# Optimization experiments

Measured on AMD Instinct MI355X. Metric: run time of the kernel, lower is better.

Reference implementation:

```python
import jax, jax.numpy as jnp
import numpy as np

B = 64            # batch of graphs
E = 8978          # edge-simplices per graph (nodes of the Hodge-1 graph)
E2 = E // 2       # after Graclus pair-pooling
K = 4             # Laguerre polynomial order
DEG = 16          # avg degree of the (edge-)adjacency
SLOPE = 0.33      # LeakyReLU negative slope
EPS = 1e-5        # BatchNorm eps


def _make_edges(rng, b, n, deg):
    # block-diagonal batched edge list: each graph only connects within itself
    offs = np.repeat(np.arange(b, dtype=np.int64) * n, n * deg)
    dst = np.tile(np.repeat(np.arange(n, dtype=np.int64), deg), b) + offs
    src = rng.integers(0, n, size=b * n * deg) + offs
    return np.stack([src, dst]).astype(np.int32)


def setup_inputs() -> dict:
    rng = np.random.default_rng(0)
    ks = jax.random.split(jax.random.key(0), 12)
    N1 = B * E
    ei1 = _make_edges(rng, B, E, DEG)
    ei2 = _make_edges(rng, B, E2, DEG)
    return {
        "x_s": jax.random.normal(ks[0], (N1, 1), jnp.float32),
        "edge_index_s": jnp.asarray(ei1),
        "edge_weight_s": jax.random.uniform(ks[1], (ei1.shape[1],), jnp.float32) * (2.0 / DEG),
        "edge_index_s1": jnp.asarray(ei2),
        "edge_weight_s1": jax.random.uniform(ks[2], (ei2.shape[1],), jnp.float32) * (2.0 / DEG),
        "W0": jax.random.normal(ks[3], (K, 1, 32), jnp.float32) * 0.3,
        "b0": jnp.zeros((32,), jnp.float32),
        "g0": jnp.ones((32,), jnp.float32),
        "be0": jnp.zeros((32,), jnp.float32),
        "W1": jax.random.normal(ks[4], (K, 32, 32), jnp.float32) * 0.1,
        "b1": jnp.zeros((32,), jnp.float32),
        "g1": jnp.ones((32,), jnp.float32),
        "be1": jnp.zeros((32,), jnp.float32),
        "W2": jax.random.normal(ks[5], (K, 32, 1), jnp.float32) * 0.1,
        "b2": jnp.zeros((1,), jnp.float32),
        "g2": jnp.ones((1,), jnp.float32),
        "be2": jnp.zeros((1,), jnp.float32),
        "lin1_W": jax.random.normal(ks[6], (E2, 256), jnp.float32) * 0.02,
        "lin1_b": jnp.zeros((256,), jnp.float32),
        "bn1_g": jnp.ones((256,), jnp.float32),
        "bn1_b": jnp.zeros((256,), jnp.float32),
        "lin2_W": jax.random.normal(ks[7], (256, 128), jnp.float32) * 0.06,
        "lin2_b": jnp.zeros((128,), jnp.float32),
        "bn2_g": jnp.ones((128,), jnp.float32),
        "bn2_b": jnp.zeros((128,), jnp.float32),
        "lin3_W": jax.random.normal(ks[8], (128, 1), jnp.float32) * 0.09,
        "lin3_b": jnp.zeros((1,), jnp.float32),
    }


def _laguerre_layer(x, src, dst, ew, W, b, gamma, beta, n):
    """HodgeLaguerreConv (K-order Laguerre recurrence over sparse L) + BatchNorm + LeakyReLU."""
    def matvec(v):  # (L v)[i] = sum_j w_ij v[j]
        return jax.ops.segment_sum(ew[:, None] * v[src], dst, num_segments=n)
    Tp = x                      # L_0(L) x = x
    out = Tp @ W[0]
    Tc = x - matvec(x)          # L_1(L) x = x - L x
    out = out + Tc @ W[1]
    for k in range(1, K - 1):   # L_{k+1} = ((2k+1-L) L_k - k L_{k-1}) / (k+1)
        Tn = ((2 * k + 1) * Tc - matvec(Tc) - k * Tp) / (k + 1)
        out = out + Tn @ W[k + 1]
        Tp, Tc = Tc, Tn
    out = out + b
    out = gamma * (out - out.mean(0)) * jax.lax.rsqrt(out.var(0) + EPS) + beta
    return jnp.where(out > 0, out, SLOPE * out)


def _bn(h, g, b):
    return g * (h - h.mean(0)) * jax.lax.rsqrt(h.var(0) + EPS) + b


def reference(x_s, edge_index_s, edge_weight_s, edge_index_s1, edge_weight_s1,
              W0, b0, g0, be0, W1, b1, g1, be1, W2, b2, g2, be2,
              lin1_W, lin1_b, bn1_g, bn1_b, lin2_W, lin2_b, bn2_g, bn2_b,
              lin3_W, lin3_b):
    N1, N2 = B * E, B * E2
    x = _laguerre_layer(x_s, edge_index_s[0], edge_index_s[1], edge_weight_s,
                        W0, b0, g0, be0, N1)
    # Graclus pooling: merge matched node pairs by max over features
    x = x.reshape(B, E2, 2, x.shape[-1]).max(axis=2).reshape(N2, -1)
    x = _laguerre_layer(x, edge_index_s1[0], edge_index_s1[1], edge_weight_s1,
                        W1, b1, g1, be1, N2)
    x = _laguerre_layer(x, edge_index_s1[0], edge_index_s1[1], edge_weight_s1,
                        W2, b2, g2, be2, N2)
    x = x.reshape(B, E2)        # last conv has 1 channel
    h = jax.nn.relu(_bn(x @ lin1_W + lin1_b, bn1_g, bn1_b))
    h = jax.nn.relu(_bn(h @ lin2_W + lin2_b, bn2_g, bn2_b))
    return h @ lin3_W + lin3_b  # [B, num_classes=1]
```

## Files before the change

### kernel.cpp

```cpp
#include <hip/hip_runtime.h>
#include <cstdint>

#define SLOPE 0.33f

static constexpr int B_   = 64;
static constexpr int E1_  = 8978;
static constexpr int E2_  = 4489;
static constexpr int N1_  = B_ * E1_;
static constexpr int N2_  = B_ * E2_;
static constexpr int DEG_ = 16;
static constexpr int QTR_ = 2245;
static constexpr int QTR2_ = 1123;
static constexpr int MVGRID = (N2_ * 32) / 256;
static constexpr int PROJ_GRID = (N2_ + 511) / 512;
static constexpr double EPS_ = 1e-5;

__device__ __forceinline__ float lrelu(float v) { return v > 0.f ? v : SLOPE * v; }
__device__ __forceinline__ float dot4(float4 a, float4 b) {
  return a.x * b.x + a.y * b.y + a.z * b.z + a.w * b.w;
}

__global__ __launch_bounds__(256) void k0_mv1(const float* __restrict__ x,
    const int* __restrict__ src, const float* __restrict__ ew, float* __restrict__ T1) {
  __shared__ float sx[E1_];
  int g = blockIdx.x >> 2, q = blockIdx.x & 3;
  int gbase = g * E1_;
  for (int j = threadIdx.x; j < E1_; j += 256) sx[j] = x[gbase + j];
  __syncthreads();
  int start = q * QTR_, end = min(start + QTR_, E1_);
  for (int i = start + (int)threadIdx.x; i < end; i += 256) {
    int node = gbase + i;
    const int4* s4 = (const int4*)(src + (size_t)node * DEG_);
    const float4* w4 = (const float4*)(ew + (size_t)node * DEG_);
    float acc = 0.f;
#pragma unroll
    for (int j = 0; j < 4; ++j) {
      int4 s = s4[j]; float4 w = w4[j];
      acc += w.x * sx[s.x - gbase] + w.y * sx[s.y - gbase]
           + w.z * sx[s.z - gbase] + w.w * sx[s.w - gbase];
    }
    T1[node] = sx[i] - acc;
  }
}

__global__ __launch_bounds__(256) void k0_mv2(const float* __restrict__ x,
    const int* __restrict__ src, const float* __restrict__ ew,
    const float* __restrict__ T1, float* __restrict__ T2) {
  __shared__ float sT[E1_];
  int g = blockIdx.x >> 2, q = blockIdx.x & 3;
  int gbase = g * E1_;
  for (int j = threadIdx.x; j < E1_; j += 256) sT[j] = T1[gbase + j];
  __syncthreads();
  int start = q * QTR_, end = min(start + QTR_, E1_);
  for (int i = start + (int)threadIdx.x; i < end; i += 256) {
    int node = gbase + i;
    const int4* s4 = (const int4*)(src + (size_t)node * DEG_);
    const float4* w4 = (const float4*)(ew + (size_t)node * DEG_);
    float acc = 0.f;
#pragma unroll
    for (int j = 0; j < 4; ++j) {
      int4 s = s4[j]; float4 w = w4[j];
      acc += w.x * sT[s.x - gbase] + w.y * sT[s.y - gbase]
           + w.z * sT[s.z - gbase] + w.w * sT[s.w - gbase];
    }
    T2[node] = (3.f * sT[i] - acc - x[node]) * 0.5f;
  }
}

__global__ __launch_bounds__(256) void k0_mv3(const float* __restrict__ x,
    const int* __restrict__ src, const float* __restrict__ ew,
    const float* __restrict__ T1, const float* __restrict__ T2,
    float* __restrict__ T3, double* mom) {
  __shared__ float sT[E1_];
  __shared__ double sred[4 * 14];
  int g = blockIdx.x >> 2, q = blockIdx.x & 3;
  int gbase = g * E1_;
  for (int j = threadIdx.x; j < E1_; j += 256) sT[j] = T2[gbase + j];
  __syncthreads();
  double m[14];
#pragma unroll
  for (int j = 0; j < 14; ++j) m[j] = 0.0;
  int start = q * QTR_, end = min(start + QTR_, E1_);
  for (int i = start + (int)threadIdx.x; i < end; i += 256) {
    int node = gbase + i;
    const int4* s4 = (const int4*)(src + (size_t)node * DEG_);
    const float4* w4 = (const float4*)(ew + (size_t)node * DEG_);
    float acc = 0.f;
#pragma unroll
    for (int j = 0; j < 4; ++j) {
      int4 s = s4[j]; float4 w = w4[j];
      acc += w.x * sT[s.x - gbase] + w.y * sT[s.y - gbase]
           + w.z * sT[s.z - gbase] + w.w * sT[s.w - gbase];
    }
    float t1 = T1[node];
    float t2 = sT[i];
    float t3 = (5.f * t2 - acc - 2.f * t1) * (1.f / 3.f);
    T3[node] = t3;
    double d0 = x[node], d1 = t1, d2 = t2, d3 = t3;
    m[0] += d0; m[1] += d1; m[2] += d2; m[3] += d3;
    m[4] += d0 * d0; m[5] += d0 * d1; m[6] += d0 * d2; m[7] += d0 * d3;
    m[8] += d1 * d1; m[9] += d1 * d2; m[10] += d1 * d3;
    m[11] += d2 * d2; m[12] += d2 * d3; m[13] += d3 * d3;
  }
  int lane = threadIdx.x & 63, wid = threadIdx.x >> 6;
#pragma unroll
  for (int j = 0; j < 14; ++j) {
    double v = m[j];
    for (int o = 32; o; o >>= 1) v += __shfl_down(v, o);
    if (lane == 0) sred[wid * 14 + j] = v;
  }
  __syncthreads();
  if (threadIdx.x < 14) {
    double s = sred[threadIdx.x] + sred[14 + threadIdx.x] + sred[28 + threadIdx.x] + sred[42 + threadIdx.x];
    atomicAdd(&mom[threadIdx.x], s);
  }
}

__global__ void k0_params(const double* __restrict__ mom, const float* __restrict__ W0,
    const float* __restrict__ g0, const float* __restrict__ be0,
    float* __restrict__ scale0, float* __restrict__ shiftE0) {
  int c = threadIdx.x;
  if (c >= 32) return;
  double inv = 1.0 / (double)N1_;
  double mm[4];
#pragma unroll
  for (int k = 0; k < 4; ++k) mm[k] = mom[k] * inv;
  double M[4][4];
  M[0][0] = mom[4] * inv;  M[0][1] = mom[5] * inv;  M[0][2] = mom[6] * inv;  M[0][3] = mom[7] * inv;
  M[1][1] = mom[8] * inv;  M[1][2] = mom[9] * inv;  M[1][3] = mom[10] * inv;
  M[2][2] = mom[11] * inv; M[2][3] = mom[12] * inv; M[3][3] = mom[13] * inv;
  M[1][0] = M[0][1]; M[2][0] = M[0][2]; M[3][0] = M[0][3];
  M[2][1] = M[1][2]; M[3][1] = M[1][3]; M[3][2] = M[2][3];
  double w[4];
#pragma unroll
  for (int k = 0; k < 4; ++k) w[k] = W0[k * 32 + c];
  double mean = 0.0;
#pragma unroll
  for (int k = 0; k < 4; ++k) mean += w[k] * mm[k];
  double e2 = 0.0;
#pragma unroll
  for (int k = 0; k < 4; ++k)
#pragma unroll
    for (int l = 0; l < 4; ++l) e2 += M[k][l] * w[k] * w[l];
  double var = e2 - mean * mean;
  double sc = (double)g0[c] / sqrt(var + EPS_);
  scale0[c] = (float)sc;
  shiftE0[c] = (float)((double)be0[c] - sc * mean);
}

__global__ __launch_bounds__(256) void k0_pool(const float* __restrict__ x,
    const float* __restrict__ T1, const float* __restrict__ T2, const float* __restrict__ T3,
    const float* __restrict__ W0, const float* __restrict__ scale0,
    const float* __restrict__ shiftE0, float* __restrict__ x1) {
  int gid = blockIdx.x * 256 + threadIdx.x;
  int grp = gid >> 5, c = gid & 31;
  if (grp >= N2_) return;
  int b = grp / E2_, j = grp - b * E2_;
  int ga = b * E1_ + 2 * j, gb = ga + 1;
  float w0 = W0[c], w1 = W0[32 + c], w2 = W0[64 + c], w3 = W0[96 + c];
  float da = x[ga] * w0 + T1[ga] * w1 + T2[ga] * w2 + T3[ga] * w3;
  float db = x[gb] * w0 + T1[gb] * w1 + T2[gb] * w2 + T3[gb] * w3;
  float sc = scale0[c], sh = shiftE0[c];
  float ya = lrelu(sc * da + sh), yb = lrelu(sc * db + sh);
  x1[grp * 32 + c] = fmaxf(ya, yb);
}

__global__ __launch_bounds__(256) void k1_projall(const float* __restrict__ X,
    const float* __restrict__ W1, float4* __restrict__ P4) {
  __shared__ float4 Wl[128 * 8];
  const float4 cfs[4] = { {0.f, 0.f, 0.f, -1.f / 6.f},
                          {0.f, 0.f, 0.5f, 1.5f},
                          {0.f, -1.f, -2.f, -3.f},
                          {1.f, 1.f, 1.f, 1.f} };
  for (int e = threadIdx.x; e < 1024; e += 256) {
    int o = e >> 3, qq = e & 7;
    int j = o >> 5, cp = o & 31;
    float4 cf = cfs[j];
    float4 w;
    {
      const float* wp = W1 + (4 * qq + 0) * 32 + cp;
      w.x = cf.x * wp[0] + cf.y * wp[1024] + cf.z * wp[2048] + cf.w * wp[3072];
    }
    {
      const float* wp = W1 + (4 * qq + 1) * 32 + cp;
      w.y = cf.x * wp[0] + cf.y * wp[1024] + cf.z * wp[2048] + cf.w * wp[3072];
    }
    {
      const float* wp = W1 + (4 * qq + 2) * 32 + cp;
      w.z = cf.x * wp[0] + cf.y * wp[1024] + cf.z * wp[2048] + cf.w * wp[3072];
    }
    {
      const float* wp = W1 + (4 * qq + 3) * 32 + cp;
      w.w = cf.x * wp[0] + cf.y * wp[1024] + cf.z * wp[2048] + cf.w * wp[3072];
    }
    Wl[e] = w;
  }
  __syncthreads();
  int rA = blockIdx.x * 512 + threadIdx.x;
  int rB = rA + 256;
  bool okA = rA < N2_, okB = rB < N2_;
  if (!okA) return;
  float4 xA[8], xB[8];
  {
    const float4* pa = (const float4*)(X + (size_t)rA * 32);
#pragma unroll
    for (int t = 0; t < 8; ++t) xA[t] = pa[t];
  }
  if (okB) {
    const float4* pb = (const float4*)(X + (size_t)rB * 32);
#pragma unroll
    for (int t = 0; t < 8; ++t) xB[t] = pb[t];
  } else {
#pragma unroll
    for (int t = 0; t < 8; ++t) xB[t] = {0.f, 0.f, 0.f, 0.f};
  }
  for (int oq = 0; oq < 32; ++oq) {
    float4 aA = {0.f, 0.f, 0.f, 0.f}, aB = {0.f, 0.f, 0.f, 0.f};
    const float4* wr = Wl + oq * 32;
#pragma unroll
    for (int qq = 0; qq < 8; ++qq) {
      float4 w0 = wr[0 * 8 + qq];
      float4 w1 = wr[1 * 8 + qq];
      float4 w2 = wr[2 * 8 + qq];
      float4 w3 = wr[3 * 8 + qq];
      float4 xa = xA[qq], xb = xB[qq];
      aA.x += dot4(xa, w0); aA.y += dot4(xa, w1); aA.z += dot4(xa, w2); aA.w += dot4(xa, w3);
      aB.x += dot4(xb, w0); aB.y += dot4(xb, w1); aB.z += dot4(xb, w2); aB.w += dot4(xb, w3);
    }
    P4[(size_t)oq * N2_ + rA] = aA;
    if (okB) P4[(size_t)oq * N2_ + rB] = aB;
  }
}

__global__ __launch_bounds__(1024) void k1_chain(const float4* __restrict__ P4,
    float4* __restrict__ O4, const int* __restrict__ src,
    const float* __restrict__ ew, double* st) {
  __shared__ float4 bA[E2_], bB[E2_];
  __shared__ float sacc[8];
  int v = (blockIdx.x & 7) * 64 + (blockIdx.x >> 3);
  int g = v >> 3, cg = v & 7;
  int gbase = g * E2_;
  int tid = threadIdx.x;
  if (tid < 8) sacc[tid] = 0.f;
  {
    const float4* sp = P4 + (size_t)cg * N2_ + gbase;
    for (int i = tid; i < E2_; i += 1024) bA[i] = sp[i];
  }
  float4* cur = bA;
  float4* nxt = bB;
  for (int s = 1; s <= 3; ++s) {
    __syncthreads();
    const float4* selfp = P4 + (size_t)(s * 8 + cg) * N2_ + gbase;
    for (int n = tid; n < E2_; n += 1024) {
      const int4* s4 = (const int4*)(src + (size_t)(gbase + n) * DEG_);
      const float4* w4 = (const float4*)(ew + (size_t)(gbase + n) * DEG_);
      float4 acc = selfp[n];
#pragma unroll
      for (int j = 0; j < 4; ++j) {
        int4 sx = s4[j]; float4 w = w4[j];
        float4 g0 = cur[sx.x - gbase];
        float4 g1 = cur[sx.y - gbase];
        float4 g2 = cur[sx.z - gbase];
        float4 g3 = cur[sx.w - gbase];
        acc.x += w.x * g0.x + w.y * g1.x + w.z * g2.x + w.w * g3.x;
        acc.y += w.x * g0.y + w.y * g1.y + w.z * g2.y + w.w * g3.y;
        acc.z += w.x * g0.z + w.y * g1.z + w.z * g2.z + w.w * g3.z;
        acc.w += w.x * g0.w + w.y * g1.w + w.z * g2.w + w.w * g3.w;
      }
      nxt[n] = acc;
    }
    float4* t = cur; cur = nxt; nxt = t;
  }
  __syncthreads();
  float4* op = O4 + (size_t)cg * N2_ + gbase;
  float4 s1 = {0.f, 0.f, 0.f, 0.f}, s2 = {0.f, 0.f, 0.f, 0.f};
  for (int n = tid; n < E2_; n += 1024) {
    float4 vv = cur[n];
    op[n] = vv;
    s1.x += vv.x; s1.y += vv.y; s1.z += vv.z; s1.w += vv.w;
    s2.x += vv.x * vv.x; s2.y += vv.y * vv.y; s2.z += vv.z * vv.z; s2.w += vv.w * vv.w;
  }
  for (int o = 32; o; o >>= 1) {
    s1.x += __shfl_down(s1.x, o); s1.y += __shfl_down(s1.y, o);
    s1.z += __shfl_down(s1.z, o); s1.w += __shfl_down(s1.w, o);
    s2.x += __shfl_down(s2.x, o); s2.y += __shfl_down(s2.y, o);
    s2.z += __shfl_down(s2.z, o); s2.w += __shfl_down(s2.w, o);
  }
  if ((tid & 63) == 0) {
    atomicAdd(&sacc[0], s1.x); atomicAdd(&sacc[1], s1.y);
    atomicAdd(&sacc[2], s1.z); atomicAdd(&sacc[3], s1.w);
    atomicAdd(&sacc[4], s2.x); atomicAdd(&sacc[5], s2.y);
    atomicAdd(&sacc[6], s2.z); atomicAdd(&sacc[7], s2.w);
  }
  __syncthreads();
  if (tid < 4) {
    int ch = cg * 4 + tid;
    atomicAdd(&st[ch], (double)sacc[tid]);
    atomicAdd(&st[32 + ch], (double)sacc[4 + tid]);
  }
}

__global__ void k1_params(const double* __restrict__ sum, const double* __restrict__ sq,
    const float* __restrict__ g1, const float* __restrict__ be1,
    float* __restrict__ scale1, float* __restrict__ shiftE1) {
  int c = threadIdx.x;
  if (c >= 32) return;
  double mean = sum[c] / (double)N2_;
  double var = sq[c] / (double)N2_ - mean * mean;
  double sc = (double)g1[c] / sqrt(var + EPS_);
  scale1[c] = (float)sc;
  shiftE1[c] = (float)((double)be1[c] - sc * mean);
}

__global__ __launch_bounds__(256) void k2_proj(const float* __restrict__ X,
    const float* __restrict__ W2, const float* __restrict__ scale1,
    const float* __restrict__ shiftE1,
    float* __restrict__ u0, float* __restrict__ u1,
    float* __restrict__ u2, float* __restrict__ u3) {
  __shared__ float qv[4][32];
  __shared__ float fsc[32], fsh[32];
  int tid = threadIdx.x;
  if (tid < 128) {
    int cp = tid & 31, j = tid >> 5;
    float w0 = W2[cp], w1 = W2[32 + cp], w2 = W2[64 + cp], w3 = W2[96 + cp];
    float q;
    if (j == 0)      q = w0 + w1 + w2 + w3;
    else if (j == 1) q = -w1 - 2.f * w2 - 3.f * w3;
    else if (j == 2) q = 0.5f * w2 + 1.5f * w3;
    else             q = -w3 * (1.f / 6.f);
    qv[j][cp] = q;
  }
  if (tid < 32) { fsc[tid] = scale1[tid]; fsh[tid] = shiftE1[tid]; }
  __syncthreads();
  int node = blockIdx.x * 256 + tid;
  if (node >= N2_) return;
  const float4* xf = (const float4*)X;
  float a0 = 0.f, a1 = 0.f, a2 = 0.f, a3 = 0.f;
#pragma unroll
  for (int t = 0; t < 8; ++t) {
    float4 v = xf[(size_t)t * N2_ + node];
    float f0 = lrelu(fsc[4 * t] * v.x + fsh[4 * t]);
    float f1 = lrelu(fsc[4 * t + 1] * v.y + fsh[4 * t + 1]);
    float f2_ = lrelu(fsc[4 * t + 2] * v.z + fsh[4 * t + 2]);
    float f3 = lrelu(fsc[4 * t + 3] * v.w + fsh[4 * t + 3]);
    a0 += f0 * qv[0][4 * t] + f1 * qv[0][4 * t + 1] + f2_ * qv[0][4 * t + 2] + f3 * qv[0][4 * t + 3];
    a1 += f0 * qv[1][4 * t] + f1 * qv[1][4 * t + 1] + f2_ * qv[1][4 * t + 2] + f3 * qv[1][4 * t + 3];
    a2 += f0 * qv[2][4 * t] + f1 * qv[2][4 * t + 1] + f2_ * qv[2][4 * t + 2] + f3 * qv[2][4 * t + 3];
    a3 += f0 * qv[3][4 * t] + f1 * qv[3][4 * t + 1] + f2_ * qv[3][4 * t + 2] + f3 * qv[3][4 * t + 3];
  }
  u0[node] = a0; u1[node] = a1; u2[node] = a2; u3[node] = a3;
}

__global__ __launch_bounds__(256) void k2_step(const float* __restrict__ z,
    const int* __restrict__ src, const float* __restrict__ ew,
    const float* __restrict__ u, float* __restrict__ zo,
    int do_stats, double* st2) {
  __shared__ float sz[E2_];
  __shared__ double sred[4][2];
  int g = blockIdx.x >> 2, q = blockIdx.x & 3;
  int gbase = g * E2_;
  for (int j = threadIdx.x; j < E2_; j += 256) sz[j] = z[gbase + j];
  __syncthreads();
  int start = q * QTR2_, end = min(start + QTR2_, E2_);
  double aS = 0.0, aQ = 0.0;
  for (int i = start + (int)threadIdx.x; i < end; i += 256) {
    int node = gbase + i;
    const int4* s4 = (const int4*)(src + (size_t)node * DEG_);
    const float4* w4 = (const float4*)(ew + (size_t)node * DEG_);
    float acc = 0.f;
#pragma unroll
    for (int j = 0; j < 4; ++j) {
      int4 s = s4[j]; float4 w = w4[j];
      acc += w.x * sz[s.x - gbase] + w.y * sz[s.y - gbase]
           + w.z * sz[s.z - gbase] + w.w * sz[s.w - gbase];
    }
    float val = u[node] + acc;
    zo[node] = val;
    if (do_stats) { aS += val; aQ += (double)val * (double)val; }
  }
  if (do_stats) {
    int lane = threadIdx.x & 63, wid = threadIdx.x >> 6;
    for (int o = 32; o; o >>= 1) { aS += __shfl_down(aS, o); aQ += __shfl_down(aQ, o); }
    if (lane == 0) { sred[wid][0] = aS; sred[wid][1] = aQ; }
    __syncthreads();
    if (threadIdx.x == 0) {
      double s = sred[0][0] + sred[1][0] + sred[2][0] + sred[3][0];
      double qq = sred[0][1] + sred[1][1] + sred[2][1] + sred[3][1];
      atomicAdd(&st2[0], s); atomicAdd(&st2[1], qq);
    }
  }
}

__global__ void k2_params(const double* __restrict__ st2, const float* __restrict__ g2,
    const float* __restrict__ be2, float* __restrict__ p ) {
  if (threadIdx.x != 0) return;
  double mean = st2[0] / (double)N2_;
  double var = st2[1] / (double)N2_ - mean * mean;
  double sc = (double)g2[0] / sqrt(var + EPS_);
  p[128] = (float)sc;
  p[129] = (float)((double)be2[0] - sc * mean);
}

__global__ __launch_bounds__(256) void k3_gemm1(const float* __restrict__ out2,
    const float* __restrict__ lin1W, const float* __restrict__ p, float* h1pre) {
  __shared__ float f2v[4][284];
  float sc = p[128], sh = p[129];
  int bs = blockIdx.x & 15, rs = blockIdx.x >> 4;
  int b0 = bs * 4;
  int r0 = rs * 281;
  int nr = min(281, E2_ - r0);
  int c = threadIdx.x;
#pragma unroll
  for (int b = 0; b < 4; ++b)
    for (int j = c; j < 284; j += 256)
      f2v[b][j] = (j < nr) ? lrelu(sc * out2[(b0 + b) * E2_ + r0 + j] + sh) : 0.f;
  __syncthreads();
  float acc0 = 0.f, acc1 = 0.f, acc2 = 0.f, acc3 = 0.f;
  int nr4 = nr & ~3;
  int j = 0;
  for (; j < nr4; j += 4) {
    const float* wp = lin1W + (size_t)(r0 + j) * 256 + c;
    float w0 = wp[0], w1 = wp[256], w2 = wp[512], w3 = wp[768];
    float4 f0 = *(const float4*)&f2v[0][j];
    float4 f1 = *(const float4*)&f2v[1][j];
    float4 f2_ = *(const float4*)&f2v[2][j];
    float4 f3 = *(const float4*)&f2v[3][j];
    acc0 += f0.x * w0 + f0.y * w1 + f0.z * w2 + f0.w * w3;
    acc1 += f1.x * w0 + f1.y * w1 + f1.z * w2 + f1.w * w3;
    acc2 += f2_.x * w0 + f2_.y * w1 + f2_.z * w2 + f2_.w * w3;
    acc3 += f3.x * w0 + f3.y * w1 + f3.z * w2 + f3.w * w3;
  }
  for (; j < nr; ++j) {
    float w = lin1W[(size_t)(r0 + j) * 256 + c];
    acc0 += f2v[0][j] * w;
    acc1 += f2v[1][j] * w;
    acc2 += f2v[2][j] * w;
    acc3 += f2v[3][j] * w;
  }
  atomicAdd(&h1pre[(b0 + 0) * 256 + c], acc0);
  atomicAdd(&h1pre[(b0 + 1) * 256 + c], acc1);
  atomicAdd(&h1pre[(b0 + 2) * 256 + c], acc2);
  atomicAdd(&h1pre[(b0 + 3) * 256 + c], acc3);
}

__global__ __launch_bounds__(256) void k4_bn1(const float* __restrict__ h1pre,
    const float* __restrict__ g, const float* __restrict__ be, float* __restrict__ h1) {
  int c = threadIdx.x;
  float vs[64];
  double s = 0.0, q = 0.0;
  for (int b = 0; b < 64; ++b) { float v = h1pre[b * 256 + c]; vs[b] = v; s += v; q += (double)v * v; }
  double mean = s / 64.0, var = q / 64.0 - mean * mean;
  double scd = (double)g[c] / sqrt(var + EPS_);
  double shd = (double)be[c] - scd * mean;
  for (int b = 0; b < 64; ++b) {
    float y = (float)(scd * vs[b] + shd);
    h1[b * 256 + c] = y > 0.f ? y : 0.f;
  }
}

__global__ __launch_bounds__(256) void k5_gemm2(const float* __restrict__ h1,
    const float* __restrict__ lin2W, float* __restrict__ h2pre) {
  __shared__ float sred[256];
  int c = blockIdx.x;
  int b = threadIdx.x & 63, q = threadIdx.x >> 6;
  float acc = 0.f;
  for (int r = q; r < 256; r += 4) acc += h1[b * 256 + r] * lin2W[r * 128 + c];
  sred[threadIdx.x] = acc;
  __syncthreads();
  if (threadIdx.x < 64)
    h2pre[threadIdx.x * 128 + c] = sred[threadIdx.x] + sred[64 + threadIdx.x]
                                 + sred[128 + threadIdx.x] + sred[192 + threadIdx.x];
}

__global__ __launch_bounds__(256) void k6_final(const float* __restrict__ h2pre,
    const float* __restrict__ g, const float* __restrict__ be,
    const float* __restrict__ W3, const float* __restrict__ b3, float* __restrict__ outp) {
  __shared__ float sh2[64 * 129];
  __shared__ float sred[256];
  int tid = threadIdx.x;
  if (tid < 128) {
    int c = tid;
    float vs[64];
    double s = 0.0, q = 0.0;
    for (int b = 0; b < 64; ++b) { float v = h2pre[b * 128 + c]; vs[b] = v; s += v; q += (double)v * v; }
    double mean = s / 64.0, var = q / 64.0 - mean * mean;
    double scd = (double)g[c] / sqrt(var + EPS_);
    double shd = (double)be[c] - scd * mean;
    for (int b = 0; b < 64; ++b) {
      float y = (float)(scd * vs[b] + shd);
      sh2[b * 129 + c] = y > 0.f ? y : 0.f;
    }
  }
  __syncthreads();
  int b = tid & 63, q = tid >> 6;
  float acc = 0.f;
  for (int r = q; r < 128; r += 4) acc += sh2[b * 129 + r] * W3[r];
  sred[tid] = acc;
  __syncthreads();
  if (tid < 64)
    outp[tid] = sred[tid] + sred[64 + tid] + sred[128 + tid] + sred[192 + tid] + b3[0];
}

extern "C" void kernel_launch(void* const* d_in, const int* in_sizes, int n_in,
                              void* d_out, int out_size, void* d_ws, size_t ws_size,
                              hipStream_t stream) {
  const float* x    = (const float*)d_in[0];
  const int*   ei1  = (const int*)d_in[1];
  const float* ew1  = (const float*)d_in[2];
  const int*   ei2  = (const int*)d_in[3];
  const float* ew2  = (const float*)d_in[4];
  const float* W0   = (const float*)d_in[5];
  const float* g0   = (const float*)d_in[7];
  const float* be0  = (const float*)d_in[8];
  const float* W1   = (const float*)d_in[9];
  const float* g1   = (const float*)d_in[11];
  const float* be1  = (const float*)d_in[12];
  const float* W2   = (const float*)d_in[13];
  const float* g2   = (const float*)d_in[15];
  const float* be2  = (const float*)d_in[16];
  const float* lin1W = (const float*)d_in[17];
  const float* bn1g = (const float*)d_in[19];
  const float* bn1b = (const float*)d_in[20];
  const float* lin2W = (const float*)d_in[21];
  const float* bn2g = (const float*)d_in[23];
  const float* bn2b = (const float*)d_in[24];
  const float* lin3W = (const float*)d_in[25];
  const float* lin3b = (const float*)d_in[26];

  char* ws = (char*)d_ws;
  double* stats  = (double*)ws;
  float*  params = (float*)(ws + 1024);
  float*  h1pre  = (float*)(ws + 4096);
  float*  h1     = (float*)(ws + 4096 + 65536);
  float*  h2pre  = (float*)(ws + 4096 + 131072);
  float*  Treg   = (float*)(ws + 262144);
  float* T1_0 = Treg;
  float* T2_0 = Treg + N1_;
  float* T3_0 = Treg + 2 * (size_t)N1_;
  float* u0   = Treg;
  float* u1   = Treg + (size_t)N2_;
  float* u2   = Treg + 2 * (size_t)N2_;
  float* u3   = Treg + 3 * (size_t)N2_;
  float* zA   = Treg + 4 * (size_t)N2_;
  float* out2 = Treg + 5 * (size_t)N2_;
  float*  big = (float*)(ws + 262144 + 3 * (size_t)N1_ * 4);
  float* bufA = big;
  float* Pbuf = big + 32 * (size_t)N2_;

  hipMemsetAsync(stats, 0, 80 * sizeof(double), stream);
  hipMemsetAsync(h1pre, 0, 65536, stream);

  k0_mv1<<<256, 256, 0, stream>>>(x, ei1, ew1, T1_0);
  k0_mv2<<<256, 256, 0, stream>>>(x, ei1, ew1, T1_0, T2_0);
  k0_mv3<<<256, 256, 0, stream>>>(x, ei1, ew1, T1_0, T2_0, T3_0, stats);
  k0_params<<<1, 32, 0, stream>>>(stats, W0, g0, be0, params, params + 32);
  k0_pool<<<MVGRID, 256, 0, stream>>>(x, T1_0, T2_0, T3_0, W0, params, params + 32, bufA);

  k1_projall<<<PROJ_GRID, 256, 0, stream>>>(bufA, W1, (float4*)Pbuf);
  k1_chain<<<512, 1024, 0, stream>>>((const float4*)Pbuf, (float4*)Pbuf, ei2, ew2, stats + 14);
  k1_params<<<1, 32, 0, stream>>>(stats + 14, stats + 46, g1, be1, params + 64, params + 96);

  k2_proj<<<(N2_ + 255) / 256, 256, 0, stream>>>(Pbuf, W2, params + 64, params + 96,
                                                 u0, u1, u2, u3);
  k2_step<<<256, 256, 0, stream>>>(u3, ei2, ew2, u2, zA, 0, nullptr);
  k2_step<<<256, 256, 0, stream>>>(zA, ei2, ew2, u1, u3, 0, nullptr);
  k2_step<<<256, 256, 0, stream>>>(u3, ei2, ew2, u0, out2, 1, stats + 78);
  k2_params<<<1, 64, 0, stream>>>(stats + 78, g2, be2, params);

  k3_gemm1<<<256, 256, 0, stream>>>(out2, lin1W, params, h1pre);
  k4_bn1<<<1, 256, 0, stream>>>(h1pre, bn1g, bn1b, h1);
  k5_gemm2<<<128, 256, 0, stream>>>(h1, lin2W, h2pre);
  k6_final<<<1, 256, 0, stream>>>(h2pre, bn2g, bn2b, lin3W, lin3b, (float*)d_out);
}
```

Measured before the change: 537.0 us.

## Compress edge indices to 16-bit local ids, single-buffer chain, resize blocks

Adds a prep kernel that converts the int32 global source indices into 16-bit graph-local indices, halving index traffic in every SpMV gather and removing the per-edge subtraction. The k1_chain kernel keeps results in registers and uses one shared buffer instead of two, cutting LDS so more blocks can be resident. The SpMV step kernels move to 1024-thread blocks and the first dense GEMM gets twice as many blocks with smaller row tiles. The cost is two extra prep kernels each call, which write into workspace buffers that are later reused.

```diff
diff --git a/kernel.cpp b/kernel.cpp
--- a/kernel.cpp
+++ b/kernel.cpp
@@ -15,83 +15,113 @@
 static constexpr int PROJ_GRID = (N2_ + 511) / 512;
 static constexpr double EPS_ = 1e-5;
 
+typedef unsigned short u16;
+typedef unsigned int   u32;
+
 __device__ __forceinline__ float lrelu(float v) { return v > 0.f ? v : SLOPE * v; }
 __device__ __forceinline__ float dot4(float4 a, float4 b) {
   return a.x * b.x + a.y * b.y + a.z * b.z + a.w * b.w;
 }
-
-__global__ __launch_bounds__(256) void k0_mv1(const float* __restrict__ x,
-    const int* __restrict__ src, const float* __restrict__ ew, float* __restrict__ T1) {
+__device__ __forceinline__ void gacc(float4& acc, float wgt, const float4& gv) {
+  acc.x += wgt * gv.x; acc.y += wgt * gv.y; acc.z += wgt * gv.z; acc.w += wgt * gv.w;
+}
+
+template<int NPG>
+__global__ __launch_bounds__(256) void k_prep(const int* __restrict__ src, int nNodes,
+    u16* __restrict__ out) {
+  int node = blockIdx.x * 256 + threadIdx.x;
+  if (node >= nNodes) return;
+  int gbase = (node / NPG) * NPG;
+  const int4* s4 = (const int4*)(src + (size_t)node * DEG_);
+  int4 a = s4[0], b = s4[1], c = s4[2], d = s4[3];
+  uint4 o0, o1;
+  o0.x = (u32)(a.x - gbase) | ((u32)(a.y - gbase) << 16);
+  o0.y = (u32)(a.z - gbase) | ((u32)(a.w - gbase) << 16);
+  o0.z = (u32)(b.x - gbase) | ((u32)(b.y - gbase) << 16);
+  o0.w = (u32)(b.z - gbase) | ((u32)(b.w - gbase) << 16);
+  o1.x = (u32)(c.x - gbase) | ((u32)(c.y - gbase) << 16);
+  o1.y = (u32)(c.z - gbase) | ((u32)(c.w - gbase) << 16);
+  o1.z = (u32)(d.x - gbase) | ((u32)(d.y - gbase) << 16);
+  o1.w = (u32)(d.z - gbase) | ((u32)(d.w - gbase) << 16);
+  uint4* op = (uint4*)(out + (size_t)node * DEG_);
+  op[0] = o0; op[1] = o1;
+}
+
+#define GATHER1(dst, sv, si_, w4_)                                              \
+  {                                                                             \
+    uint4 A_ = si_[0], Bq_ = si_[1];                                            \
+    float4 w_;                                                                  \
+    w_ = w4_[0];                                                                \
+    dst += w_.x * sv[A_.x & 0xFFFFu] + w_.y * sv[A_.x >> 16]                    \
+         + w_.z * sv[A_.y & 0xFFFFu] + w_.w * sv[A_.y >> 16];                   \
+    w_ = w4_[1];                                                                \
+    dst += w_.x * sv[A_.z & 0xFFFFu] + w_.y * sv[A_.z >> 16]                    \
+         + w_.z * sv[A_.w & 0xFFFFu] + w_.w * sv[A_.w >> 16];                   \
+    w_ = w4_[2];                                                                \
+    dst += w_.x * sv[Bq_.x & 0xFFFFu] + w_.y * sv[Bq_.x >> 16]                  \
+         + w_.z * sv[Bq_.y & 0xFFFFu] + w_.w * sv[Bq_.y >> 16];                 \
+    w_ = w4_[3];                                                                \
+    dst += w_.x * sv[Bq_.z & 0xFFFFu] + w_.y * sv[Bq_.z >> 16]                  \
+         + w_.z * sv[Bq_.w & 0xFFFFu] + w_.w * sv[Bq_.w >> 16];                 \
+  }
+
+__global__ __launch_bounds__(1024) void k0_mv1(const float* __restrict__ x,
+    const u16* __restrict__ lsrc, const float* __restrict__ ew, float* __restrict__ T1) {
   __shared__ float sx[E1_];
   int g = blockIdx.x >> 2, q = blockIdx.x & 3;
   int gbase = g * E1_;
-  for (int j = threadIdx.x; j < E1_; j += 256) sx[j] = x[gbase + j];
+  for (int j = threadIdx.x; j < E1_; j += 1024) sx[j] = x[gbase + j];
   __syncthreads();
   int start = q * QTR_, end = min(start + QTR_, E1_);
-  for (int i = start + (int)threadIdx.x; i < end; i += 256) {
+  for (int i = start + (int)threadIdx.x; i < end; i += 1024) {
     int node = gbase + i;
-    const int4* s4 = (const int4*)(src + (size_t)node * DEG_);
+    const uint4* si = (const uint4*)(lsrc + (size_t)node * DEG_);
     const float4* w4 = (const float4*)(ew + (size_t)node * DEG_);
     float acc = 0.f;
-#pragma unroll
-    for (int j = 0; j < 4; ++j) {
-      int4 s = s4[j]; float4 w = w4[j];
-      acc += w.x * sx[s.x - gbase] + w.y * sx[s.y - gbase]
-           + w.z * sx[s.z - gbase] + w.w * sx[s.w - gbase];
-    }
+    GATHER1(acc, sx, si, w4);
     T1[node] = sx[i] - acc;
   }
 }
 
-__global__ __launch_bounds__(256) void k0_mv2(const float* __restrict__ x,
-    const int* __restrict__ src, const float* __restrict__ ew,
+__global__ __launch_bounds__(1024) void k0_mv2(const float* __restrict__ x,
+    const u16* __restrict__ lsrc, const float* __restrict__ ew,
     const float* __restrict__ T1, float* __restrict__ T2) {
   __shared__ float sT[E1_];
   int g = blockIdx.x >> 2, q = blockIdx.x & 3;
   int gbase = g * E1_;
-  for (int j = threadIdx.x; j < E1_; j += 256) sT[j] = T1[gbase + j];
+  for (int j = threadIdx.x; j < E1_; j += 1024) sT[j] = T1[gbase + j];
   __syncthreads();
   int start = q * QTR_, end = min(start + QTR_, E1_);
-  for (int i = start + (int)threadIdx.x; i < end; i += 256) {
+  for (int i = start + (int)threadIdx.x; i < end; i += 1024) {
     int node = gbase + i;
-    const int4* s4 = (const int4*)(src + (size_t)node * DEG_);
+    const uint4* si = (const uint4*)(lsrc + (size_t)node * DEG_);
     const float4* w4 = (const float4*)(ew + (size_t)node * DEG_);
     float acc = 0.f;
-#pragma unroll
-    for (int j = 0; j < 4; ++j) {
-      int4 s = s4[j]; float4 w = w4[j];
-      acc += w.x * sT[s.x - gbase] + w.y * sT[s.y - gbase]
-           + w.z * sT[s.z - gbase] + w.w * sT[s.w - gbase];
-    }
+    GATHER1(acc, sT, si, w4);
     T2[node] = (3.f * sT[i] - acc - x[node]) * 0.5f;
   }
 }
 
-__global__ __launch_bounds__(256) void k0_mv3(const float* __restrict__ x,
-    const int* __restrict__ src, const float* __restrict__ ew,
+__global__ __launch_bounds__(1024) void k0_mv3(const float* __restrict__ x,
+    const u16* __restrict__ lsrc, const float* __restrict__ ew,
     const float* __restrict__ T1, const float* __restrict__ T2,
     float* __restrict__ T3, double* mom) {
   __shared__ float sT[E1_];
-  __shared__ double sred[4 * 14];
+  __shared__ double sred[16 * 14];
   int g = blockIdx.x >> 2, q = blockIdx.x & 3;
   int gbase = g * E1_;
-  for (int j = threadIdx.x; j < E1_; j += 256) sT[j] = T2[gbase + j];
+  for (int j = threadIdx.x; j < E1_; j += 1024) sT[j] = T2[gbase + j];
   __syncthreads();
   double m[14];
 #pragma unroll
   for (int j = 0; j < 14; ++j) m[j] = 0.0;
   int start = q * QTR_, end = min(start + QTR_, E1_);
-  for (int i = start + (int)threadIdx.x; i < end; i += 256) {
+  for (int i = start + (int)threadIdx.x; i < end; i += 1024) {
     int node = gbase + i;
-    const int4* s4 = (const int4*)(src + (size_t)node * DEG_);
+    const uint4* si = (const uint4*)(lsrc + (size_t)node * DEG_);
     const float4* w4 = (const float4*)(ew + (size_t)node * DEG_);
     float acc = 0.f;
-#pragma unroll
-    for (int j = 0; j < 4; ++j) {
-      int4 s = s4[j]; float4 w = w4[j];
-      acc += w.x * sT[s.x - gbase] + w.y * sT[s.y - gbase]
-           + w.z * sT[s.z - gbase] + w.w * sT[s.w - gbase];
-    }
+    GATHER1(acc, sT, si, w4);
     float t1 = T1[node];
     float t2 = sT[i];
     float t3 = (5.f * t2 - acc - 2.f * t1) * (1.f / 3.f);
@@ -111,7 +141,9 @@
   }
   __syncthreads();
   if (threadIdx.x < 14) {
-    double s = sred[threadIdx.x] + sred[14 + threadIdx.x] + sred[28 + threadIdx.x] + sred[42 + threadIdx.x];
+    double s = 0.0;
+#pragma unroll
+    for (int w = 0; w < 16; ++w) s += sred[w * 14 + threadIdx.x];
     atomicAdd(&mom[threadIdx.x], s);
   }
 }
@@ -232,10 +264,10 @@
   }
 }
 
-__global__ __launch_bounds__(1024) void k1_chain(const float4* __restrict__ P4,
-    float4* __restrict__ O4, const int* __restrict__ src,
+__global__ __launch_bounds__(1024, 8) void k1_chain(const float4* __restrict__ P4,
+    float4* __restrict__ O4, const u16* __restrict__ lsrc,
     const float* __restrict__ ew, double* st) {
-  __shared__ float4 bA[E2_], bB[E2_];
+  __shared__ float4 buf[E2_];
   __shared__ float sacc[8];
   int v = (blockIdx.x & 7) * 64 + (blockIdx.x >> 3);
   int g = v >> 3, cg = v & 7;
@@ -244,41 +276,56 @@
   if (tid < 8) sacc[tid] = 0.f;
   {
     const float4* sp = P4 + (size_t)cg * N2_ + gbase;
-    for (int i = tid; i < E2_; i += 1024) bA[i] = sp[i];
-  }
-  float4* cur = bA;
-  float4* nxt = bB;
+    for (int i = tid; i < E2_; i += 1024) buf[i] = sp[i];
+  }
+  float4 vals[5];
   for (int s = 1; s <= 3; ++s) {
     __syncthreads();
     const float4* selfp = P4 + (size_t)(s * 8 + cg) * N2_ + gbase;
-    for (int n = tid; n < E2_; n += 1024) {
-      const int4* s4 = (const int4*)(src + (size_t)(gbase + n) * DEG_);
-      const float4* w4 = (const float4*)(ew + (size_t)(gbase + n) * DEG_);
-      float4 acc = selfp[n];
-#pragma unroll
-      for (int j = 0; j < 4; ++j) {
-        int4 sx = s4[j]; float4 w = w4[j];
-        float4 g0 = cur[sx.x - gbase];
-        float4 g1 = cur[sx.y - gbase];
-        float4 g2 = cur[sx.z - gbase];
-        float4 g3 = cur[sx.w - gbase];
-        acc.x += w.x * g0.x + w.y * g1.x + w.z * g2.x + w.w * g3.x;
-        acc.y += w.x * g0.y + w.y * g1.y + w.z * g2.y + w.w * g3.y;
-        acc.z += w.x * g0.z + w.y * g1.z + w.z * g2.z + w.w * g3.z;
-        acc.w += w.x * g0.w + w.y * g1.w + w.z * g2.w + w.w * g3.w;
+#pragma unroll
+    for (int k = 0; k < 5; ++k) {
+      int n = tid + k * 1024;
+      if (n < E2_) {
+        const uint4* si = (const uint4*)(lsrc + (size_t)(gbase + n) * DEG_);
+        const float4* w4 = (const float4*)(ew + (size_t)(gbase + n) * DEG_);
+        uint4 A = si[0], Bq = si[1];
+        float4 acc = selfp[n];
+        float4 w;
+        w = w4[0];
+        gacc(acc, w.x, buf[A.x & 0xFFFFu]); gacc(acc, w.y, buf[A.x >> 16]);
+        gacc(acc, w.z, buf[A.y & 0xFFFFu]); gacc(acc, w.w, buf[A.y >> 16]);
+        w = w4[1];
+        gacc(acc, w.x, buf[A.z & 0xFFFFu]); gacc(acc, w.y, buf[A.z >> 16]);
+        gacc(acc, w.z, buf[A.w & 0xFFFFu]); gacc(acc, w.w, buf[A.w >> 16]);
+        w = w4[2];
+        gacc(acc, w.x, buf[Bq.x & 0xFFFFu]); gacc(acc, w.y, buf[Bq.x >> 16]);
+        gacc(acc, w.z, buf[Bq.y & 0xFFFFu]); gacc(acc, w.w, buf[Bq.y >> 16]);
+        w = w4[3];
+        gacc(acc, w.x, buf[Bq.z & 0xFFFFu]); gacc(acc, w.y, buf[Bq.z >> 16]);
+        gacc(acc, w.z, buf[Bq.w & 0xFFFFu]); gacc(acc, w.w, buf[Bq.w >> 16]);
+        vals[k] = acc;
       }
-      nxt[n] = acc;
-    }
-    float4* t = cur; cur = nxt; nxt = t;
-  }
-  __syncthreads();
+    }
+    if (s < 3) {
+      __syncthreads();
+#pragma unroll
+      for (int k = 0; k < 5; ++k) {
+        int n = tid + k * 1024;
+        if (n < E2_) buf[n] = vals[k];
+      }
+    }
+  }
   float4* op = O4 + (size_t)cg * N2_ + gbase;
   float4 s1 = {0.f, 0.f, 0.f, 0.f}, s2 = {0.f, 0.f, 0.f, 0.f};
-  for (int n = tid; n < E2_; n += 1024) {
-    float4 vv = cur[n];
-    op[n] = vv;
-    s1.x += vv.x; s1.y += vv.y; s1.z += vv.z; s1.w += vv.w;
-    s2.x += vv.x * vv.x; s2.y += vv.y * vv.y; s2.z += vv.z * vv.z; s2.w += vv.w * vv.w;
+#pragma unroll
+  for (int k = 0; k < 5; ++k) {
+    int n = tid + k * 1024;
+    if (n < E2_) {
+      float4 vv = vals[k];
+      op[n] = vv;
+      s1.x += vv.x; s1.y += vv.y; s1.z += vv.z; s1.w += vv.w;
+      s2.x += vv.x * vv.x; s2.y += vv.y * vv.y; s2.z += vv.z * vv.z; s2.w += vv.w * vv.w;
+    }
   }
   for (int o = 32; o; o >>= 1) {
     s1.x += __shfl_down(s1.x, o); s1.y += __shfl_down(s1.y, o);
@@ -351,29 +398,24 @@
   u0[node] = a0; u1[node] = a1; u2[node] = a2; u3[node] = a3;
 }
 
-__global__ __launch_bounds__(256) void k2_step(const float* __restrict__ z,
-    const int* __restrict__ src, const float* __restrict__ ew,
+__global__ __launch_bounds__(1024) void k2_step(const float* __restrict__ z,
+    const u16* __restrict__ lsrc, const float* __restrict__ ew,
     const float* __restrict__ u, float* __restrict__ zo,
     int do_stats, double* st2) {
   __shared__ float sz[E2_];
-  __shared__ double sred[4][2];
+  __shared__ double sred[16][2];
   int g = blockIdx.x >> 2, q = blockIdx.x & 3;
   int gbase = g * E2_;
-  for (int j = threadIdx.x; j < E2_; j += 256) sz[j] = z[gbase + j];
+  for (int j = threadIdx.x; j < E2_; j += 1024) sz[j] = z[gbase + j];
   __syncthreads();
   int start = q * QTR2_, end = min(start + QTR2_, E2_);
   double aS = 0.0, aQ = 0.0;
-  for (int i = start + (int)threadIdx.x; i < end; i += 256) {
+  for (int i = start + (int)threadIdx.x; i < end; i += 1024) {
     int node = gbase + i;
-    const int4* s4 = (const int4*)(src + (size_t)node * DEG_);
+    const uint4* si = (const uint4*)(lsrc + (size_t)node * DEG_);
     const float4* w4 = (const float4*)(ew + (size_t)node * DEG_);
     float acc = 0.f;
-#pragma unroll
-    for (int j = 0; j < 4; ++j) {
-      int4 s = s4[j]; float4 w = w4[j];
-      acc += w.x * sz[s.x - gbase] + w.y * sz[s.y - gbase]
-           + w.z * sz[s.z - gbase] + w.w * sz[s.w - gbase];
-    }
+    GATHER1(acc, sz, si, w4);
     float val = u[node] + acc;
     zo[node] = val;
     if (do_stats) { aS += val; aQ += (double)val * (double)val; }
@@ -384,8 +426,9 @@
     if (lane == 0) { sred[wid][0] = aS; sred[wid][1] = aQ; }
     __syncthreads();
     if (threadIdx.x == 0) {
-      double s = sred[0][0] + sred[1][0] + sred[2][0] + sred[3][0];
-      double qq = sred[0][1] + sred[1][1] + sred[2][1] + sred[3][1];
+      double s = 0.0, qq = 0.0;
+#pragma unroll
+      for (int w = 0; w < 16; ++w) { s += sred[w][0]; qq += sred[w][1]; }
       atomicAdd(&st2[0], s); atomicAdd(&st2[1], qq);
     }
   }
@@ -403,16 +446,16 @@
 
 __global__ __launch_bounds__(256) void k3_gemm1(const float* __restrict__ out2,
     const float* __restrict__ lin1W, const float* __restrict__ p, float* h1pre) {
-  __shared__ float f2v[4][284];
+  __shared__ float f2v[4][144];
   float sc = p[128], sh = p[129];
   int bs = blockIdx.x & 15, rs = blockIdx.x >> 4;
   int b0 = bs * 4;
-  int r0 = rs * 281;
-  int nr = min(281, E2_ - r0);
+  int r0 = rs * 141;
+  int nr = min(141, E2_ - r0);
   int c = threadIdx.x;
 #pragma unroll
   for (int b = 0; b < 4; ++b)
-    for (int j = c; j < 284; j += 256)
+    for (int j = c; j < 144; j += 256)
       f2v[b][j] = (j < nr) ? lrelu(sc * out2[(b0 + b) * E2_ + r0 + j] + sh) : 0.f;
   __syncthreads();
   float acc0 = 0.f, acc1 = 0.f, acc2 = 0.f, acc3 = 0.f;
@@ -546,28 +589,33 @@
   float*  big = (float*)(ws + 262144 + 3 * (size_t)N1_ * 4);
   float* bufA = big;
   float* Pbuf = big + 32 * (size_t)N2_;
+  u16* lsrc1 = (u16*)Pbuf;
+  u16* lsrc2 = (u16*)bufA;
 
   hipMemsetAsync(stats, 0, 80 * sizeof(double), stream);
   hipMemsetAsync(h1pre, 0, 65536, stream);
 
-  k0_mv1<<<256, 256, 0, stream>>>(x, ei1, ew1, T1_0);
-  k0_mv2<<<256, 256, 0, stream>>>(x, ei1, ew1, T1_0, T2_0);
-  k0_mv3<<<256, 256, 0, stream>>>(x, ei1, ew1, T1_0, T2_0, T3_0, stats);
+  k_prep<E1_><<<(N1_ + 255) / 256, 256, 0, stream>>>(ei1, N1_, lsrc1);
+
+  k0_mv1<<<256, 1024, 0, stream>>>(x, lsrc1, ew1, T1_0);
+  k0_mv2<<<256, 1024, 0, stream>>>(x, lsrc1, ew1, T1_0, T2_0);
+  k0_mv3<<<256, 1024, 0, stream>>>(x, lsrc1, ew1, T1_0, T2_0, T3_0, stats);
   k0_params<<<1, 32, 0, stream>>>(stats, W0, g0, be0, params, params + 32);
   k0_pool<<<MVGRID, 256, 0, stream>>>(x, T1_0, T2_0, T3_0, W0, params, params + 32, bufA);
 
   k1_projall<<<PROJ_GRID, 256, 0, stream>>>(bufA, W1, (float4*)Pbuf);
-  k1_chain<<<512, 1024, 0, stream>>>((const float4*)Pbuf, (float4*)Pbuf, ei2, ew2, stats + 14);
+  k_prep<E2_><<<(N2_ + 255) / 256, 256, 0, stream>>>(ei2, N2_, lsrc2);
+  k1_chain<<<512, 1024, 0, stream>>>((const float4*)Pbuf, (float4*)Pbuf, lsrc2, ew2, stats + 14);
   k1_params<<<1, 32, 0, stream>>>(stats + 14, stats + 46, g1, be1, params + 64, params + 96);
 
   k2_proj<<<(N2_ + 255) / 256, 256, 0, stream>>>(Pbuf, W2, params + 64, params + 96,
                                                  u0, u1, u2, u3);
-  k2_step<<<256, 256, 0, stream>>>(u3, ei2, ew2, u2, zA, 0, nullptr);
-  k2_step<<<256, 256, 0, stream>>>(zA, ei2, ew2, u1, u3, 0, nullptr);
-  k2_step<<<256, 256, 0, stream>>>(u3, ei2, ew2, u0, out2, 1, stats + 78);
+  k2_step<<<256, 1024, 0, stream>>>(u3, lsrc2, ew2, u2, zA, 0, nullptr);
+  k2_step<<<256, 1024, 0, stream>>>(zA, lsrc2, ew2, u1, u3, 0, nullptr);
+  k2_step<<<256, 1024, 0, stream>>>(u3, lsrc2, ew2, u0, out2, 1, stats + 78);
   k2_params<<<1, 64, 0, stream>>>(stats + 78, g2, be2, params);
 
-  k3_gemm1<<<256, 256, 0, stream>>>(out2, lin1W, params, h1pre);
+  k3_gemm1<<<512, 256, 0, stream>>>(out2, lin1W, params, h1pre);
   k4_bn1<<<1, 256, 0, stream>>>(h1pre, bn1g, bn1b, h1);
   k5_gemm2<<<128, 256, 0, stream>>>(h1, lin2W, h2pre);
   k6_final<<<1, 256, 0, stream>>>(h2pre, bn2g, bn2b, lin3W, lin3b, (float*)d_out);
```

Measured after the change: 1.626 ms. +202.9%, slower.
